# Performance work log

Hardware: AMD Instinct MI355X
Metric: run time of the kernel (lower is better)

The kernel has to match this reference:

```python
import jax, jax.numpy as jnp
import numpy as np


def _bilinear_resize_nchw(x, out_h, out_w):
    """Torch F.interpolate(mode='bilinear', align_corners=False), no antialias."""
    B, C, H, W = x.shape

    def coords(out_n, in_n):
        src = jnp.maximum(0.0, (jnp.arange(out_n, dtype=jnp.float32) + 0.5) * (in_n / out_n) - 0.5)
        f = jnp.floor(src)
        i0 = jnp.clip(f.astype(jnp.int32), 0, in_n - 1)
        i1 = jnp.clip(i0 + 1, 0, in_n - 1)
        frac = src - f
        return i0, i1, frac

    y0, y1, fy = coords(out_h, H)
    x0, x1, fx = coords(out_w, W)
    rows = x[:, :, y0, :] * (1.0 - fy)[None, None, :, None] + x[:, :, y1, :] * fy[None, None, :, None]
    out = rows[:, :, :, x0] * (1.0 - fx)[None, None, None, :] + rows[:, :, :, x1] * fx[None, None, None, :]
    return out


def setup_inputs() -> dict:
    key = jax.random.key(0)
    k1, k2, k3, k4 = jax.random.split(key, 4)
    return {
        "query_value": jax.random.normal(k1, (2, 256, 64, 128), dtype=jnp.float32),
        "memory_keys_low": jax.random.normal(k2, (2, 4, 64, 32, 64), dtype=jnp.float32),
        "memory_values_low": jax.random.normal(k3, (2, 4, 256, 32, 64), dtype=jnp.float32),
        "query_key_low": jax.random.normal(k4, (2, 64, 32, 64), dtype=jnp.float32),
    }


def reference(query_value, memory_keys_low, memory_values_low, query_key_low):
    B, T, Ck, H, W = memory_keys_low.shape
    Cv = memory_values_low.shape[2]
    # keys: BxTxCkxHxW -> Bx(T*H*W)xCk via permute(0,2,1,3,4)+view+permute
    mk = jnp.transpose(memory_keys_low, (0, 2, 1, 3, 4)).reshape(B, Ck, T * H * W)
    qk = query_key_low.reshape(B, Ck, H * W)
    # attn[b, m, n] over memory locations m (softmax axis), query locations n
    attn = jnp.einsum('bcm,bcn->bmn', mk, qk)  # [B, T*H*W, H*W]
    # matmul_norm=False: no key_channels**-0.5 scaling
    attn = jax.nn.softmax(attn, axis=1)
    mv = jnp.transpose(memory_values_low, (0, 2, 1, 3, 4)).reshape(B, Cv, T * H * W)
    memory = jnp.einsum('bcm,bmn->bcn', mv, attn).reshape(B, Cv, H, W)
    qv = _bilinear_resize_nchw(query_value, H, W)
    return jnp.concatenate([qv, memory], axis=1)  # [B, 2*Cv, H, W]
```

## Files before the change

kernel.cpp:

```cpp
#include <hip/hip_runtime.h>
#include <cstdint>

#define BATCH 2
#define TT    4
#define CKD   64
#define CVD   256
#define NQ    2048
#define MM    8192
#define TQ    64
#define TM    32
#define MSPLIT 8
#define MCHUNK (MM / MSPLIT)
#define NIT    (MCHUNK / TM)

typedef unsigned short u16;
typedef __bf16 bf16x8 __attribute__((ext_vector_type(8)));
typedef float  f32x4  __attribute__((ext_vector_type(4)));

struct __attribute__((aligned(8)))  U16x4 { u16 x, y, z, w; };
struct __attribute__((aligned(16))) U16x8 { u16 v[8]; };

__device__ __forceinline__ u16 f2bf(float x) {
    uint32_t u = __float_as_uint(x);
    uint32_t r = (u + 0x7FFFu + ((u >> 16) & 1u)) >> 16;
    return (u16)r;
}
__device__ __forceinline__ float bf2f(u16 h) {
    return __uint_as_float(((uint32_t)h) << 16);
}

#define MFMA(a, b, c) __builtin_amdgcn_mfma_f32_16x16x32_bf16((a), (b), (c), 0, 0, 0)

#define WS_VB   0u
#define WS_KHI  8388608u
#define WS_KLO  10485760u
#define WS_QHI  12582912u
#define WS_QLO  13107200u
#define WS_LP   13631488u
#define WS_UP   13893632u

__global__ __launch_bounds__(256)
void prep_fused(const float* __restrict__ qv, const float* __restrict__ mk,
                const float* __restrict__ qk, const float* __restrict__ mv,
                float* __restrict__ out, u16* __restrict__ vb,
                u16* __restrict__ khi, u16* __restrict__ klo,
                u16* __restrict__ qhi, u16* __restrict__ qlo) {
    __shared__ float tile[64 * 65];
    const int bid = blockIdx.x;
    const int tid = threadIdx.x;

    if (bid < 4096) {
        int idx = bid * 256 + tid;
        int n  = idx & 2047;
        int bc = idx >> 11;
        int x = n & 63, y = n >> 6;
        const float* ib = qv + (size_t)bc * (64 * 128) + (2 * y) * 128 + 2 * x;
        float2 r0 = *(const float2*)ib;
        float2 r1 = *(const float2*)(ib + 128);
        int b = bc >> 8, c = bc & 255;
        out[((size_t)(b * 512 + c)) * NQ + n] = 0.25f * (r0.x + r0.y + r1.x + r1.y);
    } else if (bid < 6144) {
        int idx = (bid - 4096) * 256 + tid;
        const float4* s = (const float4*)mv + (size_t)idx * 2;
        float4 a = s[0], b = s[1];
        U16x8 o;
        o.v[0] = f2bf(a.x); o.v[1] = f2bf(a.y); o.v[2] = f2bf(a.z); o.v[3] = f2bf(a.w);
        o.v[4] = f2bf(b.x); o.v[5] = f2bf(b.y); o.v[6] = f2bf(b.z); o.v[7] = f2bf(b.w);
        *(U16x8*)(vb + (size_t)idx * 8) = o;
    } else {
        const float* src;
        u16 *dhi, *dlo;
        int blk;
        if (bid < 6400) { src = mk; dhi = khi; dlo = klo; blk = bid - 6144; }
        else            { src = qk; dhi = qhi; dlo = qlo; blk = bid - 6400; }
        const int g  = blk >> 5;
        const int mg = blk & 31;
        const float* s = src + (size_t)g * 64 * 2048 + mg * 64;

        const int c = tid >> 2;
        const int q = tid & 3;
        #pragma unroll
        for (int i = 0; i < 4; ++i) {
            float4 v = *(const float4*)(s + (size_t)c * 2048 + q * 16 + i * 4);
            int m = q * 16 + i * 4;
            tile[(m + 0) * 65 + c] = v.x;
            tile[(m + 1) * 65 + c] = v.y;
            tile[(m + 2) * 65 + c] = v.z;
            tile[(m + 3) * 65 + c] = v.w;
        }
        __syncthreads();

        const int mo = tid >> 2;
        const int cb = (tid & 3) * 16;
        U16x8 h0, h1, l0, l1;
        #pragma unroll
        for (int j = 0; j < 8; ++j) {
            float v = tile[mo * 65 + cb + j];
            u16 h = f2bf(v);
            h0.v[j] = h; l0.v[j] = f2bf(v - bf2f(h));
            float v2 = tile[mo * 65 + cb + 8 + j];
            u16 h2 = f2bf(v2);
            h1.v[j] = h2; l1.v[j] = f2bf(v2 - bf2f(h2));
        }
        size_t o = ((size_t)g * 2048 + mg * 64 + mo) * 64 + cb;
        *(U16x8*)(dhi + o) = h0; *(U16x8*)(dhi + o + 8) = h1;
        *(U16x8*)(dlo + o) = l0; *(U16x8*)(dlo + o + 8) = l1;
    }
}

__global__ __launch_bounds__(256, 2)
void flash_attn(const u16* __restrict__ khi_g, const u16* __restrict__ klo_g,
                const u16* __restrict__ vb_g, const u16* __restrict__ qhi_g,
                const u16* __restrict__ qlo_g, float* __restrict__ Up,
                float* __restrict__ Lp) {
    __shared__ __align__(16) u16 smem[2][17408];

    const int tid    = threadIdx.x;
    const int bx     = blockIdx.x;
    const int mchunk = bx & 7;
    const int ntile  = (bx >> 3) & 31;
    const int b      = bx >> 8;

    const int lane = tid & 63;
    const int w    = tid >> 6;
    const int quad = lane >> 4;
    const int l15  = lane & 15;

    const int bt      = b * TT + (mchunk >> 1);
    const int hw_base = (mchunk & 1) * MCHUNK;

    bf16x8 qh[2][2], ql[2][2];
    {
        const int nbase = ntile * TQ + (w >> 1) * 32;
        #pragma unroll
        for (int nsi = 0; nsi < 2; ++nsi) {
            size_t o = ((size_t)(b * NQ + nbase + nsi * 16 + l15)) * 64 + quad * 8;
            qh[nsi][0] = *(const bf16x8*)&qhi_g[o];
            qh[nsi][1] = *(const bf16x8*)&qhi_g[o + 32];
            ql[nsi][0] = *(const bf16x8*)&qlo_g[o];
            ql[nsi][1] = *(const bf16x8*)&qlo_g[o + 32];
        }
    }

    const u16* kh_base = khi_g + ((size_t)bt * 2048 + hw_base) * 64;
    const u16* kl_base = klo_g + ((size_t)bt * 2048 + hw_base) * 64;
    const u16* v_base  = vb_g + (size_t)bt * CVD * 2048 + hw_base;

    f32x4 O[2][8];
    #pragma unroll
    for (int i = 0; i < 2; ++i)
        #pragma unroll
        for (int j = 0; j < 8; ++j)
            O[i][j] = (f32x4){0.f, 0.f, 0.f, 0.f};
    float Lloc[2] = {0.f, 0.f};

    const int msub     = w & 1;
    const int nsubpair = w >> 1;
    const int npair    = w & 1;
    const int chalf    = w >> 1;

    const int km = tid >> 3;
    const int kc = (tid & 7) * 8;
    const int vc = tid >> 2;
    const int vm = (tid & 3) * 8;

    bf16x8 kh_r = *(const bf16x8*)&kh_base[(size_t)km * 64 + kc];
    bf16x8 kl_r = *(const bf16x8*)&kl_base[(size_t)km * 64 + kc];
    bf16x8 v_r[4];
    #pragma unroll
    for (int p = 0; p < 4; ++p)
        v_r[p] = *(const bf16x8*)&v_base[(size_t)(vc + p * 64) * 2048 + vm];

    #pragma unroll 2
    for (int it = 0; it < NIT; ++it) {
        u16* Khi = smem[it & 1];
        u16* Klo = Khi + 2304;
        u16* Vs  = Khi + 4608;
        u16* Ps  = Khi + 14848;

        *(bf16x8*)&Khi[km * 72 + kc] = kh_r;
        *(bf16x8*)&Klo[km * 72 + kc] = kl_r;
        #pragma unroll
        for (int p = 0; p < 4; ++p)
            *(bf16x8*)&Vs[(vc + p * 64) * 40 + vm] = v_r[p];
        __syncthreads();

        f32x4 acc[2];
        acc[0] = (f32x4){0.f, 0.f, 0.f, 0.f};
        acc[1] = (f32x4){0.f, 0.f, 0.f, 0.f};
        #pragma unroll
        for (int ks = 0; ks < 2; ++ks) {
            bf16x8 ah = *(const bf16x8*)&Khi[(msub * 16 + l15) * 72 + ks * 32 + quad * 8];
            bf16x8 al = *(const bf16x8*)&Klo[(msub * 16 + l15) * 72 + ks * 32 + quad * 8];
            #pragma unroll
            for (int nsi = 0; nsi < 2; ++nsi) {
                acc[nsi] = MFMA(ah, qh[nsi][ks], acc[nsi]);
                acc[nsi] = MFMA(ah, ql[nsi][ks], acc[nsi]);
                acc[nsi] = MFMA(al, qh[nsi][ks], acc[nsi]);
            }
        }
        #pragma unroll
        for (int nsi = 0; nsi < 2; ++nsi) {
            int n = (nsubpair * 2 + nsi) * 16 + l15;
            float p0 = __expf(acc[nsi][0]);
            float p1 = __expf(acc[nsi][1]);
            float p2 = __expf(acc[nsi][2]);
            float p3 = __expf(acc[nsi][3]);
            Lloc[nsi] += (p0 + p1) + (p2 + p3);
            U16x4 pk = {f2bf(p0), f2bf(p1), f2bf(p2), f2bf(p3)};
            *(U16x4*)&Ps[n * 40 + msub * 16 + quad * 4] = pk;
        }
        __syncthreads();

        if (it + 1 < NIT) {
            const int hw1 = (it + 1) * TM;
            kh_r = *(const bf16x8*)&kh_base[(size_t)(hw1 + km) * 64 + kc];
            kl_r = *(const bf16x8*)&kl_base[(size_t)(hw1 + km) * 64 + kc];
            #pragma unroll
            for (int p = 0; p < 4; ++p)
                v_r[p] = *(const bf16x8*)&v_base[(size_t)(vc + p * 64) * 2048 + hw1 + vm];
        }

        bf16x8 a2[2];
        #pragma unroll
        for (int nsi2 = 0; nsi2 < 2; ++nsi2)
            a2[nsi2] = *(const bf16x8*)&Ps[(npair * 32 + nsi2 * 16 + l15) * 40 + quad * 8];
        #pragma unroll
        for (int cs = 0; cs < 8; ++cs) {
            bf16x8 bv = *(const bf16x8*)&Vs[(chalf * 128 + cs * 16 + l15) * 40 + quad * 8];
            O[0][cs] = MFMA(a2[0], bv, O[0][cs]);
            O[1][cs] = MFMA(a2[1], bv, O[1][cs]);
        }
    }

    #pragma unroll
    for (int nsi = 0; nsi < 2; ++nsi) {
        float v = Lloc[nsi];
        v += __shfl_xor(v, 16);
        v += __shfl_xor(v, 32);
        if (quad == nsi) {
            int nsub = nsubpair * 2 + nsi;
            Lp[(((size_t)mchunk * 2 + msub) * BATCH + b) * NQ + ntile * TQ + nsub * 16 + l15] = v;
        }
    }

    float* ubase = Up + (((size_t)mchunk * BATCH + b) * NQ + ntile * TQ) * CVD
                 + (size_t)(npair * 32) * CVD + chalf * 128;
    #pragma unroll
    for (int nsi2 = 0; nsi2 < 2; ++nsi2) {
        #pragma unroll
        for (int cs = 0; cs < 8; ++cs) {
            #pragma unroll
            for (int r = 0; r < 4; ++r) {
                int n_local = nsi2 * 16 + quad * 4 + r;
                ubase[(size_t)n_local * CVD + cs * 16 + l15] = O[nsi2][cs][r];
            }
        }
    }
}

__global__ __launch_bounds__(256) void reduce_div(const float* __restrict__ Up,
                                                  const float* __restrict__ Lp,
                                                  float* __restrict__ out) {
    __shared__ float lds[16 * 65];
    const int tid = threadIdx.x;
    const int cq  = blockIdx.x & 3;
    const int n0  = ((blockIdx.x >> 2) & 127) * 16;
    const int b   = blockIdx.x >> 9;

    const int n_local = tid >> 4;
    const int c_loc   = (tid & 15) * 4;
    const int c       = cq * 64 + c_loc;

    float4 acc = {0.f, 0.f, 0.f, 0.f};
    for (int ms = 0; ms < MSPLIT; ++ms) {
        float4 v = *(const float4*)(Up + (((size_t)ms * BATCH + b) * NQ + n0 + n_local) * CVD + c);
        acc.x += v.x; acc.y += v.y; acc.z += v.z; acc.w += v.w;
    }

    float Lsum = 0.f;
    #pragma unroll
    for (int s = 0; s < MSPLIT * 2; ++s)
        Lsum += Lp[((size_t)s * BATCH + b) * NQ + n0 + n_local];
    const float inv = 1.0f / Lsum;

    lds[n_local * 65 + c_loc + 0] = acc.x * inv;
    lds[n_local * 65 + c_loc + 1] = acc.y * inv;
    lds[n_local * 65 + c_loc + 2] = acc.z * inv;
    lds[n_local * 65 + c_loc + 3] = acc.w * inv;
    __syncthreads();

    const int c_out = tid >> 2;
    const int nq    = (tid & 3) * 4;
    float4 v;
    v.x = lds[(nq + 0) * 65 + c_out];
    v.y = lds[(nq + 1) * 65 + c_out];
    v.z = lds[(nq + 2) * 65 + c_out];
    v.w = lds[(nq + 3) * 65 + c_out];
    *(float4*)(out + ((size_t)(b * 512 + 256 + cq * 64 + c_out)) * NQ + n0 + nq) = v;
}

extern "C" void kernel_launch(void* const* d_in, const int* in_sizes, int n_in,
                              void* d_out, int out_size, void* d_ws, size_t ws_size,
                              hipStream_t stream) {
    const float* qv = (const float*)d_in[0];
    const float* mk = (const float*)d_in[1];
    const float* mv = (const float*)d_in[2];
    const float* qk = (const float*)d_in[3];
    float* out = (float*)d_out;

    u16*   vb  = (u16*)((char*)d_ws + WS_VB);
    u16*   khi = (u16*)((char*)d_ws + WS_KHI);
    u16*   klo = (u16*)((char*)d_ws + WS_KLO);
    u16*   qhi = (u16*)((char*)d_ws + WS_QHI);
    u16*   qlo = (u16*)((char*)d_ws + WS_QLO);
    float* Lp  = (float*)((char*)d_ws + WS_LP);
    float* Up  = (float*)((char*)d_ws + WS_UP);

    prep_fused<<<6464, 256, 0, stream>>>(qv, mk, qk, mv, out, vb, khi, klo, qhi, qlo);
    flash_attn<<<512, 256, 0, stream>>>(khi, klo, vb, qhi, qlo, Up, Lp);
    reduce_div<<<1024, 256, 0, stream>>>(Up, Lp, out);
}
```

Before: 133.6 us.

## Load V fragments directly from global into registers, dropping the V LDS tile

Each wave now owns 64 value channels for all 64 query rows and loads its V MFMA operand fragments straight from global memory into registers, double-buffered across iterations. The V staging in shared memory is removed, which shrinks LDS from about 68KB to 28KB per block and removes the V store and load traffic. The trade-off is more strided, less coalesced global loads (16-byte chunks per row of a 2048-wide array) and more P fragment reads per wave, plus extra registers for the v_next buffer.

```diff
diff --git a/kernel.cpp b/kernel.cpp
--- a/kernel.cpp
+++ b/kernel.cpp
@@ -113,7 +113,7 @@
                 const u16* __restrict__ vb_g, const u16* __restrict__ qhi_g,
                 const u16* __restrict__ qlo_g, float* __restrict__ Up,
                 float* __restrict__ Lp) {
-    __shared__ __align__(16) u16 smem[2][17408];
+    __shared__ __align__(16) u16 smem[2][7168];
 
     const int tid    = threadIdx.x;
     const int bx     = blockIdx.x;
@@ -144,45 +144,38 @@
 
     const u16* kh_base = khi_g + ((size_t)bt * 2048 + hw_base) * 64;
     const u16* kl_base = klo_g + ((size_t)bt * 2048 + hw_base) * 64;
-    const u16* v_base  = vb_g + (size_t)bt * CVD * 2048 + hw_base;
-
-    f32x4 O[2][8];
-    #pragma unroll
-    for (int i = 0; i < 2; ++i)
-        #pragma unroll
-        for (int j = 0; j < 8; ++j)
+    const u16* v_frag_base = vb_g + (size_t)bt * CVD * 2048 + hw_base
+                           + (size_t)(w * 64 + l15) * 2048 + quad * 8;
+
+    f32x4 O[4][4];
+    #pragma unroll
+    for (int i = 0; i < 4; ++i)
+        #pragma unroll
+        for (int j = 0; j < 4; ++j)
             O[i][j] = (f32x4){0.f, 0.f, 0.f, 0.f};
     float Lloc[2] = {0.f, 0.f};
 
     const int msub     = w & 1;
     const int nsubpair = w >> 1;
-    const int npair    = w & 1;
-    const int chalf    = w >> 1;
 
     const int km = tid >> 3;
     const int kc = (tid & 7) * 8;
-    const int vc = tid >> 2;
-    const int vm = (tid & 3) * 8;
 
     bf16x8 kh_r = *(const bf16x8*)&kh_base[(size_t)km * 64 + kc];
     bf16x8 kl_r = *(const bf16x8*)&kl_base[(size_t)km * 64 + kc];
-    bf16x8 v_r[4];
-    #pragma unroll
-    for (int p = 0; p < 4; ++p)
-        v_r[p] = *(const bf16x8*)&v_base[(size_t)(vc + p * 64) * 2048 + vm];
+    bf16x8 v_cur[4], v_next[4];
+    #pragma unroll
+    for (int cs = 0; cs < 4; ++cs)
+        v_cur[cs] = *(const bf16x8*)&v_frag_base[(size_t)(cs * 16) * 2048];
 
     #pragma unroll 2
     for (int it = 0; it < NIT; ++it) {
         u16* Khi = smem[it & 1];
         u16* Klo = Khi + 2304;
-        u16* Vs  = Khi + 4608;
-        u16* Ps  = Khi + 14848;
+        u16* Ps  = Khi + 4608;
 
         *(bf16x8*)&Khi[km * 72 + kc] = kh_r;
         *(bf16x8*)&Klo[km * 72 + kc] = kl_r;
-        #pragma unroll
-        for (int p = 0; p < 4; ++p)
-            *(bf16x8*)&Vs[(vc + p * 64) * 40 + vm] = v_r[p];
         __syncthreads();
 
         f32x4 acc[2];
@@ -217,20 +210,23 @@
             kh_r = *(const bf16x8*)&kh_base[(size_t)(hw1 + km) * 64 + kc];
             kl_r = *(const bf16x8*)&kl_base[(size_t)(hw1 + km) * 64 + kc];
             #pragma unroll
-            for (int p = 0; p < 4; ++p)
-                v_r[p] = *(const bf16x8*)&v_base[(size_t)(vc + p * 64) * 2048 + hw1 + vm];
-        }
-
-        bf16x8 a2[2];
-        #pragma unroll
-        for (int nsi2 = 0; nsi2 < 2; ++nsi2)
-            a2[nsi2] = *(const bf16x8*)&Ps[(npair * 32 + nsi2 * 16 + l15) * 40 + quad * 8];
-        #pragma unroll
-        for (int cs = 0; cs < 8; ++cs) {
-            bf16x8 bv = *(const bf16x8*)&Vs[(chalf * 128 + cs * 16 + l15) * 40 + quad * 8];
-            O[0][cs] = MFMA(a2[0], bv, O[0][cs]);
-            O[1][cs] = MFMA(a2[1], bv, O[1][cs]);
-        }
+            for (int cs = 0; cs < 4; ++cs)
+                v_next[cs] = *(const bf16x8*)&v_frag_base[(size_t)(cs * 16) * 2048 + hw1];
+        }
+
+        bf16x8 a2[4];
+        #pragma unroll
+        for (int nsub = 0; nsub < 4; ++nsub)
+            a2[nsub] = *(const bf16x8*)&Ps[(nsub * 16 + l15) * 40 + quad * 8];
+        #pragma unroll
+        for (int cs = 0; cs < 4; ++cs)
+            #pragma unroll
+            for (int nsub = 0; nsub < 4; ++nsub)
+                O[nsub][cs] = MFMA(a2[nsub], v_cur[cs], O[nsub][cs]);
+
+        #pragma unroll
+        for (int cs = 0; cs < 4; ++cs)
+            v_cur[cs] = v_next[cs];
     }
 
     #pragma unroll
@@ -244,16 +240,15 @@
         }
     }
 
-    float* ubase = Up + (((size_t)mchunk * BATCH + b) * NQ + ntile * TQ) * CVD
-                 + (size_t)(npair * 32) * CVD + chalf * 128;
-    #pragma unroll
-    for (int nsi2 = 0; nsi2 < 2; ++nsi2) {
-        #pragma unroll
-        for (int cs = 0; cs < 8; ++cs) {
+    float* ubase = Up + (((size_t)mchunk * BATCH + b) * NQ + ntile * TQ) * CVD + w * 64;
+    #pragma unroll
+    for (int nsub = 0; nsub < 4; ++nsub) {
+        #pragma unroll
+        for (int cs = 0; cs < 4; ++cs) {
             #pragma unroll
             for (int r = 0; r < 4; ++r) {
-                int n_local = nsi2 * 16 + quad * 4 + r;
-                ubase[(size_t)n_local * CVD + cs * 16 + l15] = O[nsi2][cs][r];
+                int n_local = nsub * 16 + quad * 4 + r;
+                ubase[(size_t)n_local * CVD + cs * 16 + l15] = O[nsub][cs][r];
             }
         }
     }
```

Result: no change. 134.6 us (+0.8%).
